# Kernel optimization log

Measured on AMD Instinct MI355X. Metric: run time of the kernel, lower is better.

Reference implementation:

```python
import jax, jax.numpy as jnp
import numpy as np

EPS = 1e-12

def _l2(v):
    return v / (jnp.linalg.norm(v) + EPS)

def _sn_weight(w, u):
    # Spectral normalization, one power iteration with stored u (not updated here).
    cout = w.shape[-1]
    wm = w.reshape(-1, cout)              # [d, cout]
    u = jax.lax.stop_gradient(u)
    v = _l2(wm @ u)                       # [d]
    u2 = _l2(wm.T @ v)                    # [cout]
    sigma = v @ (wm @ u2)
    return w / sigma

def _conv1x1(x, w, u):
    # 1x1 conv, no bias, with spectral-normalized kernel. x: [B,H,W,Cin], w: [1,1,Cin,Cout]
    wbar = _sn_weight(w, u)[0, 0]         # [Cin, Cout]
    return jnp.einsum('bhwc,co->bhwo', x, wbar)

def _maxpool2(x):
    # 2x2 max pool, stride 2, valid. x: [B,H,W,C]
    B, H, W, C = x.shape
    return x.reshape(B, H // 2, 2, W // 2, 2, C).max(axis=(2, 4))

def setup_inputs() -> dict:
    key = jax.random.key(0)
    ks = jax.random.split(key, 9)
    B, H, W, C = 16, 64, 64, 64
    inp = {
        'x': jax.random.normal(ks[0], (B, H, W, C), jnp.float32),
        'w_theta': jax.random.normal(ks[1], (1, 1, C, C // 8), jnp.float32) * 0.05,
        'u_theta': jax.random.normal(ks[2], (C // 8,), jnp.float32),
        'w_phi': jax.random.normal(ks[3], (1, 1, C, C // 8), jnp.float32) * 0.05,
        'u_phi': jax.random.normal(ks[4], (C // 8,), jnp.float32),
        'w_g': jax.random.normal(ks[5], (1, 1, C, C // 2), jnp.float32) * 0.05,
        'u_g': jax.random.normal(ks[6], (C // 2,), jnp.float32),
        'w_o': jax.random.normal(ks[7], (1, 1, C // 2, C), jnp.float32) * 0.05,
        'u_o': jax.random.normal(ks[8], (C,), jnp.float32),
        'gamma': jnp.zeros((1,), jnp.float32),
    }
    return inp

def reference(x, w_theta, u_theta, w_phi, u_phi, w_g, u_g, w_o, u_o, gamma):
    B, H, W, C = x.shape
    theta = _conv1x1(x, w_theta, u_theta).reshape(B, H * W, C // 8)          # [B,HW,C/8]
    phi = _maxpool2(_conv1x1(x, w_phi, u_phi)).reshape(B, H * W // 4, C // 8)  # [B,HW/4,C/8]
    attn = jax.nn.softmax(jnp.einsum('bnk,bmk->bnm', theta, phi), axis=-1)   # [B,HW,HW/4]
    g = _maxpool2(_conv1x1(x, w_g, u_g)).reshape(B, H * W // 4, C // 2)      # [B,HW/4,C/2]
    attn_g = jnp.einsum('bnm,bmc->bnc', attn, g).reshape(B, H, W, C // 2)    # [B,H,W,C/2]
    attn_g = _conv1x1(attn_g, w_o, u_o)                                      # [B,H,W,C]
    return x + gamma * attn_g
```

## Files before the change

kernel.cpp:

```cpp
#include <hip/hip_runtime.h>
#include <hip/hip_bf16.h>
#include <math.h>

#define NB 16
#define NPIX 4096
#define MPOOL 1024

typedef __attribute__((ext_vector_type(8))) short bf16x8;
typedef __attribute__((ext_vector_type(4))) float f32x4;

#define LOG2E 1.44269504088896340736f

__device__ inline unsigned short f2bf(float f) {
    __hip_bfloat16 h = __float2bfloat16(f);
    return *reinterpret_cast<unsigned short*>(&h);
}

#if defined(__has_builtin)
#if __has_builtin(__builtin_amdgcn_cvt_pk_bf16_f32)
#define HAVE_PK_BF16 1
#endif
#endif
__device__ inline unsigned pack_bf16(float a, float b) {
#ifdef HAVE_PK_BF16
    typedef __bf16 bf16v2 __attribute__((ext_vector_type(2)));
    bf16v2 v = __builtin_amdgcn_cvt_pk_bf16_f32(a, b);
    unsigned u;
    __builtin_memcpy(&u, &v, 4);
    return u;
#else
    unsigned ua = __float_as_uint(a) + 0x8000u;
    unsigned ub = __float_as_uint(b) + 0x8000u;
    return __builtin_amdgcn_perm(ua, ub, 0x03020706u);
#endif
}


__device__ inline float wave_sum64(float v) {
    #pragma unroll
    for (int off = 32; off >= 1; off >>= 1) v += __shfl_xor(v, off);
    return v;
}

template<int D, int COUT>
__device__ float sn_inv_sigma(const float* __restrict__ w, const float* __restrict__ u) {
    const int lane = threadIdx.x & 63;
    float vi = 0.f;
    if (lane < D) {
        #pragma unroll 8
        for (int j = 0; j < COUT; ++j) vi += w[lane * COUT + j] * u[j];
    }
    float nn = wave_sum64(vi * vi);
    vi *= 1.0f / (sqrtf(nn) + 1e-12f);

    float u2 = 0.f;
    #pragma unroll 8
    for (int i = 0; i < D; ++i) {
        float vv = __shfl(vi, i);
        if (lane < COUT) u2 += w[i * COUT + lane] * vv;
    }
    float nn2 = wave_sum64(u2 * u2);
    u2 *= 1.0f / (sqrtf(nn2) + 1e-12f);

    float ti = 0.f;
    #pragma unroll 8
    for (int j = 0; j < COUT; ++j) {
        float uv = __shfl(u2, j);
        if (lane < D) ti += w[lane * COUT + j] * uv;
    }
    float sig = wave_sum64(vi * ti);
    return 1.0f / sig;
}

__global__ __launch_bounds__(256) void conv_all_kernel(const float* __restrict__ x,
                                                       const float* __restrict__ w_theta, const float* __restrict__ u_theta,
                                                       const float* __restrict__ w_phi,   const float* __restrict__ u_phi,
                                                       const float* __restrict__ w_g,     const float* __restrict__ u_g,
                                                       const float* __restrict__ w_o,     const float* __restrict__ u_o,
                                                       unsigned short* __restrict__ theta_bf,
                                                       unsigned short* __restrict__ phi_bf,
                                                       unsigned short* __restrict__ gT_bf,
                                                       unsigned short* __restrict__ woT_bf) {
    __shared__ unsigned short sx[128 * 72];
    __shared__ unsigned short sw[48 * 72];
    __shared__ float s_inv[3];

    const int tid  = threadIdx.x;
    const int b    = blockIdx.x >> 5;
    const int hp   = blockIdx.x & 31;
    const int h0   = hp * 2;
    const int wv   = tid >> 6;
    const int lane = tid & 63;
    const int quad = lane >> 4;
    const int lcol = lane & 15;
    const int w0   = wv * 16;

    const float4* xb4 = (const float4*)(x + (((size_t)b * NPIX) + h0 * 64) * 64);
    #pragma unroll
    for (int it = 0; it < 8; ++it) {
        const int li = tid + it * 256;
        float4 v = xb4[li];
        const int px = li >> 4, c4 = li & 15;
        uint2 pk;
        pk.x = pack_bf16(v.x, v.y);
        pk.y = pack_bf16(v.z, v.w);
        *(uint2*)(&sx[px * 72 + c4 * 4]) = pk;
    }
    if (wv == 0)      { float iv = sn_inv_sigma<64, 8>(w_theta, u_theta); if (lane == 0) s_inv[0] = iv; }
    else if (wv == 1) { float iv = sn_inv_sigma<64, 8>(w_phi,   u_phi);   if (lane == 0) s_inv[1] = iv; }
    else if (wv == 2) { float iv = sn_inv_sigma<64, 32>(w_g,    u_g);     if (lane == 0) s_inv[2] = iv; }
    else if (blockIdx.x == 0) {
        float iv = sn_inv_sigma<32, 64>(w_o, u_o);
        for (int idx = lane; idx < 64 * 32; idx += 64) {
            const int n = idx >> 5, k = idx & 31;
            woT_bf[idx] = f2bf(w_o[k * 64 + n] * iv);
        }
    }
    __syncthreads();

    {
        const float i0 = s_inv[0], i1 = s_inv[1], i2 = s_inv[2];
        #pragma unroll
        for (int it = 0; it < 12; ++it) {
            const int idx = tid + it * 256;
            const int col = idx >> 6, k = idx & 63;
            float wvf, inv;
            if (col < 8)       { wvf = w_theta[k * 8 + col];        inv = i0; }
            else if (col < 16) { wvf = w_phi[k * 8 + (col - 8)];    inv = i1; }
            else               { wvf = w_g[k * 32 + (col - 16)];    inv = i2; }
            sw[col * 72 + k] = f2bf(wvf * inv);
        }
    }
    __syncthreads();

    bf16x8 a[2][2];
    #pragma unroll
    for (int hh = 0; hh < 2; ++hh)
        #pragma unroll
        for (int kc = 0; kc < 2; ++kc)
            a[hh][kc] = *(const bf16x8*)(sx + (hh * 64 + w0 + lcol) * 72 + kc * 32 + quad * 8);

    f32x4 acc[2][3];
    #pragma unroll
    for (int ct = 0; ct < 3; ++ct) {
        bf16x8 b0 = *(const bf16x8*)(sw + (ct * 16 + lcol) * 72 + 0 * 32 + quad * 8);
        bf16x8 b1 = *(const bf16x8*)(sw + (ct * 16 + lcol) * 72 + 1 * 32 + quad * 8);
        #pragma unroll
        for (int hh = 0; hh < 2; ++hh) {
            f32x4 c = __builtin_amdgcn_mfma_f32_16x16x32_bf16(a[hh][0], b0, (f32x4)0.0f, 0, 0, 0);
            acc[hh][ct] = __builtin_amdgcn_mfma_f32_16x16x32_bf16(a[hh][1], b1, c, 0, 0, 0);
        }
    }
    __syncthreads();

    unsigned short* th = sx;
    unsigned short* ph = sx + 1024;
    unsigned short* gg = sx + 1280;
    const int ml = (w0 >> 1) + quad * 2;
    if (lcol < 8) {
        #pragma unroll
        for (int hh = 0; hh < 2; ++hh) {
            const int pix = hh * 64 + w0 + quad * 4;
            #pragma unroll
            for (int r = 0; r < 4; ++r)
                th[(pix + r) * 8 + lcol] = f2bf(acc[hh][0][r] * LOG2E);
        }
    } else {
        #pragma unroll
        for (int r2 = 0; r2 < 2; ++r2) {
            float pe = fmaxf(fmaxf(acc[0][0][2 * r2], acc[0][0][2 * r2 + 1]),
                             fmaxf(acc[1][0][2 * r2], acc[1][0][2 * r2 + 1]));
            ph[(ml + r2) * 8 + (lcol - 8)] = f2bf(pe);
        }
    }
    #pragma unroll
    for (int ct = 1; ct < 3; ++ct) {
        const int cg = (ct - 1) * 16 + lcol;
        #pragma unroll
        for (int r2 = 0; r2 < 2; ++r2) {
            float pe = fmaxf(fmaxf(acc[0][ct][2 * r2], acc[0][ct][2 * r2 + 1]),
                             fmaxf(acc[1][ct][2 * r2], acc[1][ct][2 * r2 + 1]));
            gg[cg * 32 + ml + r2] = f2bf(pe);
        }
    }
    __syncthreads();

    const float4* sv4 = (const float4*)sx;
    float4* th4 = (float4*)(theta_bf + ((size_t)b * NPIX + hp * 128) * 8);
    float4* ph4 = (float4*)(phi_bf + ((size_t)b * MPOOL + hp * 32) * 8);
    for (int idx = tid; idx < 288; idx += 256) {
        float4 v = sv4[idx];
        if (idx < 128) {
            th4[idx] = v;
        } else if (idx < 160) {
            ph4[idx - 128] = v;
        } else {
            const int gi = idx - 160;
            const int ch = gi >> 2, part = gi & 3;
            *(float4*)(gT_bf + ((size_t)b * 32 + ch) * MPOOL + hp * 32 + part * 8) = v;
        }
    }
}

__global__ __launch_bounds__(512) void attn_kernel(const unsigned short* __restrict__ theta_bf,
                                                   const unsigned short* __restrict__ phi_bf,
                                                   const unsigned short* __restrict__ gT_bf,
                                                   const unsigned short* __restrict__ woT_bf,
                                                   const float* __restrict__ x,
                                                   const float* __restrict__ gamma,
                                                   float* __restrict__ out) {
    __shared__ unsigned short sphi[MPOOL * 8];
    __shared__ unsigned short sg[2][32 * 264];
    __shared__ unsigned short sP[8][16 * 72];
    __shared__ unsigned short swo[64 * 40];

    const int tid  = threadIdx.x;
    const int b    = blockIdx.x >> 5;
    const int qb   = blockIdx.x & 31;
    const int w    = tid >> 6;
    const int lane = tid & 63;
    const int quad = lane >> 4;
    const int lcol = lane & 15;

    {
        const float4* src = (const float4*)(phi_bf + (size_t)b * (MPOOL * 8));
        float4* dst = (float4*)sphi;
        dst[2 * tid]     = src[2 * tid];
        dst[2 * tid + 1] = src[2 * tid + 1];
    }
    {
        const int n = tid >> 3, ks = (tid & 7) * 4;
        *(uint2*)(swo + n * 40 + ks) = *(const uint2*)(woT_bf + n * 32 + ks);
    }
    const unsigned short* gTb = gT_bf + (size_t)b * (32 * MPOOL);
    const int prow = tid >> 4, pseg = tid & 15;
    {
        const float4* src = (const float4*)(gTb + prow * MPOOL + pseg * 16);
        float4 r0 = src[0], r1 = src[1];
        float4* dst = (float4*)(&sg[0][prow * 264 + pseg * 16]);
        dst[0] = r0; dst[1] = r1;
    }
    const int q0w = qb * 128 + w * 16;
    bf16x8 tfrag = (bf16x8)(short)0;
    if (quad == 0)
        tfrag = *(const bf16x8*)(theta_bf + ((size_t)b * NPIX + q0w + lcol) * 8);
    __syncthreads();

    f32x4 olo = (f32x4)0.0f, ohi = (f32x4)0.0f;
    float ls = 0.f;
    unsigned short* sPw = sP[w];

    float4 pre0, pre1;
    for (int t = 0; t < 4; ++t) {
        if (t < 3) {
            const float4* src = (const float4*)(gTb + prow * MPOOL + (t + 1) * 256 + pseg * 16);
            pre0 = src[0]; pre1 = src[1];
        }
        const unsigned short* sgb = sg[t & 1];
        for (int cb = 0; cb < 4; ++cb) {
            const int m0 = t * 256 + cb * 64;
            f32x4 s[4];
            #pragma unroll
            for (int sc = 0; sc < 4; ++sc) {
                bf16x8 pf = *(const bf16x8*)(sphi + (size_t)(m0 + sc * 16 + lcol) * 8);
                s[sc] = __builtin_amdgcn_mfma_f32_16x16x32_bf16(pf, tfrag, (f32x4)0.0f, 0, 0, 0);
            }
            #pragma unroll
            for (int sc = 0; sc < 4; ++sc) {
                float e0 = exp2f(s[sc][0]);
                float e1 = exp2f(s[sc][1]);
                float e2 = exp2f(s[sc][2]);
                float e3 = exp2f(s[sc][3]);
                ls += (e0 + e1) + (e2 + e3);
                uint2 pk2;
                pk2.x = pack_bf16(e0, e1);
                pk2.y = pack_bf16(e2, e3);
                *(uint2*)(sPw + lcol * 72 + sc * 16 + quad * 4) = pk2;
            }
            asm volatile("s_waitcnt lgkmcnt(0)" ::: "memory");
            #pragma unroll
            for (int pkk = 0; pkk < 2; ++pkk) {
                bf16x8 afrag = *(const bf16x8*)(sPw + lcol * 72 + pkk * 32 + quad * 8);
                bf16x8 bg0 = *(const bf16x8*)(sgb + lcol * 264 + cb * 64 + pkk * 32 + quad * 8);
                olo = __builtin_amdgcn_mfma_f32_16x16x32_bf16(afrag, bg0, olo, 0, 0, 0);
                bf16x8 bg1 = *(const bf16x8*)(sgb + (16 + lcol) * 264 + cb * 64 + pkk * 32 + quad * 8);
                ohi = __builtin_amdgcn_mfma_f32_16x16x32_bf16(afrag, bg1, ohi, 0, 0, 0);
            }
        }
        if (t < 3) {
            float4* dst = (float4*)(&sg[(t + 1) & 1][prow * 264 + pseg * 16]);
            dst[0] = pre0; dst[1] = pre1;
        }
        __syncthreads();
    }

    ls += __shfl_xor(ls, 16);
    ls += __shfl_xor(ls, 32);
    const float invq = 1.0f / ls;

    #pragma unroll
    for (int r = 0; r < 4; ++r) {
        sPw[(quad * 4 + r) * 40 + lcol]      = f2bf(olo[r]);
        sPw[(quad * 4 + r) * 40 + 16 + lcol] = f2bf(ohi[r]);
    }
    asm volatile("s_waitcnt lgkmcnt(0)" ::: "memory");
    bf16x8 agf = *(const bf16x8*)(sPw + lcol * 40 + quad * 8);

    const float gmi = gamma[0] * invq;
    const size_t pixbase = ((size_t)b * NPIX + q0w + lcol) * 64;
    #pragma unroll
    for (int ct = 0; ct < 4; ++ct) {
        bf16x8 wa = *(const bf16x8*)(swo + (ct * 16 + lcol) * 40 + quad * 8);
        f32x4 oc = __builtin_amdgcn_mfma_f32_16x16x32_bf16(wa, agf, (f32x4)0.0f, 0, 0, 0);
        const float4 xv = *(const float4*)(x + pixbase + ct * 16 + quad * 4);
        float4 ov;
        ov.x = xv.x + gmi * oc[0];
        ov.y = xv.y + gmi * oc[1];
        ov.z = xv.z + gmi * oc[2];
        ov.w = xv.w + gmi * oc[3];
        *(float4*)(out + pixbase + ct * 16 + quad * 4) = ov;
    }
}

extern "C" void kernel_launch(void* const* d_in, const int* in_sizes, int n_in,
                              void* d_out, int out_size, void* d_ws, size_t ws_size,
                              hipStream_t stream) {
    const float* x       = (const float*)d_in[0];
    const float* w_theta = (const float*)d_in[1];
    const float* u_theta = (const float*)d_in[2];
    const float* w_phi   = (const float*)d_in[3];
    const float* u_phi   = (const float*)d_in[4];
    const float* w_g     = (const float*)d_in[5];
    const float* u_g     = (const float*)d_in[6];
    const float* w_o     = (const float*)d_in[7];
    const float* u_o     = (const float*)d_in[8];
    const float* gamma   = (const float*)d_in[9];
    float* out = (float*)d_out;

    unsigned short* u16base  = (unsigned short*)d_ws;
    unsigned short* theta_bf = u16base;
    unsigned short* phi_bf   = u16base + 524288;
    unsigned short* gT_bf    = u16base + 655360;
    unsigned short* woT_bf   = u16base + 1179648;

    conv_all_kernel<<<512, 256, 0, stream>>>(x, w_theta, u_theta, w_phi, u_phi, w_g, u_g,
                                             w_o, u_o, theta_bf, phi_bf, gT_bf, woT_bf);
    attn_kernel<<<512, 512, 0, stream>>>(theta_bf, phi_bf, gT_bf, woT_bf, x, gamma, out);
}
```

Before: 120.4 us.

## Switch attention to 32x32x16 MFMA with permlane P reuse and full-g LDS

Rewrites the attention kernel to use 32x32x16 bf16 MFMA tiles, with 32 queries per wave and 256 queries per block, launching half as many blocks. The softmax probabilities go straight from the score accumulator into the PV MFMA operand through v_permlane32_swap, which drops the per-wave LDS round-trip for P. The whole g^T for the batch now loads into LDS at once instead of being double-buffered, and the output projection also uses 32x32 MFMAs. In exchange, the block uses more LDS, the grid of 256 blocks may underfill the GPU, and the big up-front g load is no longer overlapped with compute.

```diff
diff --git a/kernel.cpp b/kernel.cpp
--- a/kernel.cpp
+++ b/kernel.cpp
@@ -8,6 +8,7 @@
 
 typedef __attribute__((ext_vector_type(8))) short bf16x8;
 typedef __attribute__((ext_vector_type(4))) float f32x4;
+typedef __attribute__((ext_vector_type(16))) float f32x16;
 
 #define LOG2E 1.44269504088896340736f
 
@@ -210,17 +211,17 @@
                                                    const float* __restrict__ gamma,
                                                    float* __restrict__ out) {
     __shared__ unsigned short sphi[MPOOL * 8];
-    __shared__ unsigned short sg[2][32 * 264];
-    __shared__ unsigned short sP[8][16 * 72];
+    __shared__ unsigned short sg[32][1032];
     __shared__ unsigned short swo[64 * 40];
+    __shared__ unsigned short strans[8][32 * 40];
 
     const int tid  = threadIdx.x;
-    const int b    = blockIdx.x >> 5;
-    const int qb   = blockIdx.x & 31;
-    const int w    = tid >> 6;
+    const int b    = blockIdx.x >> 4;
+    const int qb   = blockIdx.x & 15;
+    const int wv   = tid >> 6;
     const int lane = tid & 63;
-    const int quad = lane >> 4;
-    const int lcol = lane & 15;
+    const int l31  = lane & 31;
+    const int half = lane >> 5;
 
     {
         const float4* src = (const float4*)(phi_bf + (size_t)b * (MPOOL * 8));
@@ -232,93 +233,84 @@
         const int n = tid >> 3, ks = (tid & 7) * 4;
         *(uint2*)(swo + n * 40 + ks) = *(const uint2*)(woT_bf + n * 32 + ks);
     }
-    const unsigned short* gTb = gT_bf + (size_t)b * (32 * MPOOL);
-    const int prow = tid >> 4, pseg = tid & 15;
     {
-        const float4* src = (const float4*)(gTb + prow * MPOOL + pseg * 16);
-        float4 r0 = src[0], r1 = src[1];
-        float4* dst = (float4*)(&sg[0][prow * 264 + pseg * 16]);
-        dst[0] = r0; dst[1] = r1;
-    }
-    const int q0w = qb * 128 + w * 16;
+        const unsigned short* gTb = gT_bf + (size_t)b * (32 * MPOOL);
+        const int r = tid >> 4, seg = tid & 15;
+        const float4* src = (const float4*)(gTb + r * MPOOL + seg * 64);
+        float4* dst = (float4*)(&sg[r][seg * 64]);
+        #pragma unroll
+        for (int j = 0; j < 8; ++j) dst[j] = src[j];
+    }
+    const int q0w = qb * 256 + wv * 32;
     bf16x8 tfrag = (bf16x8)(short)0;
-    if (quad == 0)
-        tfrag = *(const bf16x8*)(theta_bf + ((size_t)b * NPIX + q0w + lcol) * 8);
-    __syncthreads();
-
-    f32x4 olo = (f32x4)0.0f, ohi = (f32x4)0.0f;
+    if (half == 0)
+        tfrag = *(const bf16x8*)(theta_bf + ((size_t)b * NPIX + q0w + l31) * 8);
+    __syncthreads();
+
+    f32x16 acc = (f32x16)0.0f;
     float ls = 0.f;
-    unsigned short* sPw = sP[w];
-
-    float4 pre0, pre1;
-    for (int t = 0; t < 4; ++t) {
-        if (t < 3) {
-            const float4* src = (const float4*)(gTb + prow * MPOOL + (t + 1) * 256 + pseg * 16);
-            pre0 = src[0]; pre1 = src[1];
-        }
-        const unsigned short* sgb = sg[t & 1];
-        for (int cb = 0; cb < 4; ++cb) {
-            const int m0 = t * 256 + cb * 64;
-            f32x4 s[4];
-            #pragma unroll
-            for (int sc = 0; sc < 4; ++sc) {
-                bf16x8 pf = *(const bf16x8*)(sphi + (size_t)(m0 + sc * 16 + lcol) * 8);
-                s[sc] = __builtin_amdgcn_mfma_f32_16x16x32_bf16(pf, tfrag, (f32x4)0.0f, 0, 0, 0);
-            }
-            #pragma unroll
-            for (int sc = 0; sc < 4; ++sc) {
-                float e0 = exp2f(s[sc][0]);
-                float e1 = exp2f(s[sc][1]);
-                float e2 = exp2f(s[sc][2]);
-                float e3 = exp2f(s[sc][3]);
-                ls += (e0 + e1) + (e2 + e3);
-                uint2 pk2;
-                pk2.x = pack_bf16(e0, e1);
-                pk2.y = pack_bf16(e2, e3);
-                *(uint2*)(sPw + lcol * 72 + sc * 16 + quad * 4) = pk2;
-            }
-            asm volatile("s_waitcnt lgkmcnt(0)" ::: "memory");
-            #pragma unroll
-            for (int pkk = 0; pkk < 2; ++pkk) {
-                bf16x8 afrag = *(const bf16x8*)(sPw + lcol * 72 + pkk * 32 + quad * 8);
-                bf16x8 bg0 = *(const bf16x8*)(sgb + lcol * 264 + cb * 64 + pkk * 32 + quad * 8);
-                olo = __builtin_amdgcn_mfma_f32_16x16x32_bf16(afrag, bg0, olo, 0, 0, 0);
-                bf16x8 bg1 = *(const bf16x8*)(sgb + (16 + lcol) * 264 + cb * 64 + pkk * 32 + quad * 8);
-                ohi = __builtin_amdgcn_mfma_f32_16x16x32_bf16(afrag, bg1, ohi, 0, 0, 0);
-            }
-        }
-        if (t < 3) {
-            float4* dst = (float4*)(&sg[(t + 1) & 1][prow * 264 + pseg * 16]);
-            dst[0] = pre0; dst[1] = pre1;
-        }
-        __syncthreads();
-    }
-
-    ls += __shfl_xor(ls, 16);
+
+    for (int mt = 0; mt < 32; ++mt) {
+        const int m0 = mt * 32;
+        bf16x8 pa = *(const bf16x8*)(sphi + (size_t)(m0 + l31) * 8);
+        f32x16 S = __builtin_amdgcn_mfma_f32_32x32x16_bf16(pa, tfrag, (f32x16)0.0f, 0, 0, 0);
+        float e0  = exp2f(S[0]),  e1  = exp2f(S[1]),  e2  = exp2f(S[2]),  e3  = exp2f(S[3]);
+        float e4  = exp2f(S[4]),  e5  = exp2f(S[5]),  e6  = exp2f(S[6]),  e7  = exp2f(S[7]);
+        float e8  = exp2f(S[8]),  e9  = exp2f(S[9]),  e10 = exp2f(S[10]), e11 = exp2f(S[11]);
+        float e12 = exp2f(S[12]), e13 = exp2f(S[13]), e14 = exp2f(S[14]), e15 = exp2f(S[15]);
+        ls += (((e0 + e1) + (e2 + e3)) + ((e4 + e5) + (e6 + e7)))
+            + (((e8 + e9) + (e10 + e11)) + ((e12 + e13) + (e14 + e15)));
+        unsigned c0 = pack_bf16(e0, e1),   c1 = pack_bf16(e2, e3);
+        unsigned c2 = pack_bf16(e4, e5),   c3 = pack_bf16(e6, e7);
+        unsigned c4 = pack_bf16(e8, e9),   c5 = pack_bf16(e10, e11);
+        unsigned c6 = pack_bf16(e12, e13), c7 = pack_bf16(e14, e15);
+        asm("v_permlane32_swap_b32 %0, %1" : "+v"(c2), "+v"(c0));
+        asm("v_permlane32_swap_b32 %0, %1" : "+v"(c3), "+v"(c1));
+        asm("v_permlane32_swap_b32 %0, %1" : "+v"(c6), "+v"(c4));
+        asm("v_permlane32_swap_b32 %0, %1" : "+v"(c7), "+v"(c5));
+        unsigned f0[4] = {c0, c1, c2, c3};
+        bf16x8 p0; __builtin_memcpy(&p0, f0, 16);
+        bf16x8 gb0 = *(const bf16x8*)(&sg[l31][m0 + half * 8]);
+        acc = __builtin_amdgcn_mfma_f32_32x32x16_bf16(p0, gb0, acc, 0, 0, 0);
+        unsigned f1[4] = {c4, c5, c6, c7};
+        bf16x8 p1; __builtin_memcpy(&p1, f1, 16);
+        bf16x8 gb1 = *(const bf16x8*)(&sg[l31][m0 + 16 + half * 8]);
+        acc = __builtin_amdgcn_mfma_f32_32x32x16_bf16(p1, gb1, acc, 0, 0, 0);
+    }
+
     ls += __shfl_xor(ls, 32);
     const float invq = 1.0f / ls;
 
-    #pragma unroll
-    for (int r = 0; r < 4; ++r) {
-        sPw[(quad * 4 + r) * 40 + lcol]      = f2bf(olo[r]);
-        sPw[(quad * 4 + r) * 40 + 16 + lcol] = f2bf(ohi[r]);
+    unsigned short* st = &strans[wv][0];
+    #pragma unroll
+    for (int r = 0; r < 16; ++r) {
+        const int q = (r & 3) + 8 * (r >> 2) + 4 * half;
+        st[q * 40 + l31] = f2bf(acc[r]);
     }
     asm volatile("s_waitcnt lgkmcnt(0)" ::: "memory");
-    bf16x8 agf = *(const bf16x8*)(sPw + lcol * 40 + quad * 8);
 
     const float gmi = gamma[0] * invq;
-    const size_t pixbase = ((size_t)b * NPIX + q0w + lcol) * 64;
-    #pragma unroll
-    for (int ct = 0; ct < 4; ++ct) {
-        bf16x8 wa = *(const bf16x8*)(swo + (ct * 16 + lcol) * 40 + quad * 8);
-        f32x4 oc = __builtin_amdgcn_mfma_f32_16x16x32_bf16(wa, agf, (f32x4)0.0f, 0, 0, 0);
-        const float4 xv = *(const float4*)(x + pixbase + ct * 16 + quad * 4);
-        float4 ov;
-        ov.x = xv.x + gmi * oc[0];
-        ov.y = xv.y + gmi * oc[1];
-        ov.z = xv.z + gmi * oc[2];
-        ov.w = xv.w + gmi * oc[3];
-        *(float4*)(out + pixbase + ct * 16 + quad * 4) = ov;
+    const size_t pixbase = ((size_t)b * NPIX + q0w + l31) * 64;
+    #pragma unroll
+    for (int ct = 0; ct < 2; ++ct) {
+        f32x16 oc = (f32x16)0.0f;
+        #pragma unroll
+        for (int kc = 0; kc < 2; ++kc) {
+            bf16x8 wa = *(const bf16x8*)(swo + (ct * 32 + l31) * 40 + kc * 16 + half * 8);
+            bf16x8 ag = *(const bf16x8*)(st + l31 * 40 + kc * 16 + half * 8);
+            oc = __builtin_amdgcn_mfma_f32_32x32x16_bf16(wa, ag, oc, 0, 0, 0);
+        }
+        #pragma unroll
+        for (int r2 = 0; r2 < 4; ++r2) {
+            const int co = ct * 32 + 8 * r2 + 4 * half;
+            const float4 xv = *(const float4*)(x + pixbase + co);
+            float4 ov;
+            ov.x = xv.x + gmi * oc[4 * r2 + 0];
+            ov.y = xv.y + gmi * oc[4 * r2 + 1];
+            ov.z = xv.z + gmi * oc[4 * r2 + 2];
+            ov.w = xv.w + gmi * oc[4 * r2 + 3];
+            *(float4*)(out + pixbase + co) = ov;
+        }
     }
 }
 
@@ -345,5 +337,5 @@
 
     conv_all_kernel<<<512, 256, 0, stream>>>(x, w_theta, u_theta, w_phi, u_phi, w_g, u_g,
                                              w_o, u_o, theta_bf, phi_bf, gT_bf, woT_bf);
-    attn_kernel<<<512, 512, 0, stream>>>(theta_bf, phi_bf, gT_bf, woT_bf, x, gamma, out);
-}
+    attn_kernel<<<256, 512, 0, stream>>>(theta_bf, phi_bf, gT_bf, woT_bf, x, gamma, out);
+}
```

After: 122.2 us. No clear change (+1.5%).

## Use 1024-thread attention blocks with single-buffered g tile and global w_o reads

Applied to the files above, without the earlier changes.

Doubles the attention block to 16 waves covering 256 queries, so each batch's phi and g tiles are staged into shared memory by half as many blocks. The g tile goes from double-buffered to single-buffered, with two barriers per step around the refill. The w_o shared staging is removed and its fragments are read straight from global memory. This cuts redundant staging traffic and LDS footprint, but adds barrier stalls and leaves only 256 blocks to spread across the CUs.

```diff
diff --git a/kernel.cpp b/kernel.cpp
--- a/kernel.cpp
+++ b/kernel.cpp
@@ -202,21 +202,20 @@
     }
 }
 
-__global__ __launch_bounds__(512) void attn_kernel(const unsigned short* __restrict__ theta_bf,
-                                                   const unsigned short* __restrict__ phi_bf,
-                                                   const unsigned short* __restrict__ gT_bf,
-                                                   const unsigned short* __restrict__ woT_bf,
-                                                   const float* __restrict__ x,
-                                                   const float* __restrict__ gamma,
-                                                   float* __restrict__ out) {
+__global__ __launch_bounds__(1024) void attn_kernel(const unsigned short* __restrict__ theta_bf,
+                                                    const unsigned short* __restrict__ phi_bf,
+                                                    const unsigned short* __restrict__ gT_bf,
+                                                    const unsigned short* __restrict__ woT_bf,
+                                                    const float* __restrict__ x,
+                                                    const float* __restrict__ gamma,
+                                                    float* __restrict__ out) {
     __shared__ unsigned short sphi[MPOOL * 8];
-    __shared__ unsigned short sg[2][32 * 264];
-    __shared__ unsigned short sP[8][16 * 72];
-    __shared__ unsigned short swo[64 * 40];
+    __shared__ unsigned short sg[32 * 264];
+    __shared__ unsigned short sP[16][16 * 72];
 
     const int tid  = threadIdx.x;
-    const int b    = blockIdx.x >> 5;
-    const int qb   = blockIdx.x & 31;
+    const int b    = blockIdx.x >> 4;
+    const int qb   = blockIdx.x & 15;
     const int w    = tid >> 6;
     const int lane = tid & 63;
     const int quad = lane >> 4;
@@ -224,23 +223,15 @@
 
     {
         const float4* src = (const float4*)(phi_bf + (size_t)b * (MPOOL * 8));
-        float4* dst = (float4*)sphi;
-        dst[2 * tid]     = src[2 * tid];
-        dst[2 * tid + 1] = src[2 * tid + 1];
-    }
+        ((float4*)sphi)[tid] = src[tid];
+    }
+    const unsigned short* gTb = gT_bf + (size_t)b * (32 * MPOOL);
+    const int gr = tid >> 5, gseg = tid & 31;
     {
-        const int n = tid >> 3, ks = (tid & 7) * 4;
-        *(uint2*)(swo + n * 40 + ks) = *(const uint2*)(woT_bf + n * 32 + ks);
-    }
-    const unsigned short* gTb = gT_bf + (size_t)b * (32 * MPOOL);
-    const int prow = tid >> 4, pseg = tid & 15;
-    {
-        const float4* src = (const float4*)(gTb + prow * MPOOL + pseg * 16);
-        float4 r0 = src[0], r1 = src[1];
-        float4* dst = (float4*)(&sg[0][prow * 264 + pseg * 16]);
-        dst[0] = r0; dst[1] = r1;
-    }
-    const int q0w = qb * 128 + w * 16;
+        *(float4*)(&sg[gr * 264 + gseg * 8]) =
+            *(const float4*)(gTb + gr * MPOOL + gseg * 8);
+    }
+    const int q0w = qb * 256 + w * 16;
     bf16x8 tfrag = (bf16x8)(short)0;
     if (quad == 0)
         tfrag = *(const bf16x8*)(theta_bf + ((size_t)b * NPIX + q0w + lcol) * 8);
@@ -250,13 +241,10 @@
     float ls = 0.f;
     unsigned short* sPw = sP[w];
 
-    float4 pre0, pre1;
     for (int t = 0; t < 4; ++t) {
-        if (t < 3) {
-            const float4* src = (const float4*)(gTb + prow * MPOOL + (t + 1) * 256 + pseg * 16);
-            pre0 = src[0]; pre1 = src[1];
-        }
-        const unsigned short* sgb = sg[t & 1];
+        float4 pre;
+        if (t < 3)
+            pre = *(const float4*)(gTb + gr * MPOOL + (t + 1) * 256 + gseg * 8);
         for (int cb = 0; cb < 4; ++cb) {
             const int m0 = t * 256 + cb * 64;
             f32x4 s[4];
@@ -281,17 +269,17 @@
             #pragma unroll
             for (int pkk = 0; pkk < 2; ++pkk) {
                 bf16x8 afrag = *(const bf16x8*)(sPw + lcol * 72 + pkk * 32 + quad * 8);
-                bf16x8 bg0 = *(const bf16x8*)(sgb + lcol * 264 + cb * 64 + pkk * 32 + quad * 8);
+                bf16x8 bg0 = *(const bf16x8*)(sg + lcol * 264 + cb * 64 + pkk * 32 + quad * 8);
                 olo = __builtin_amdgcn_mfma_f32_16x16x32_bf16(afrag, bg0, olo, 0, 0, 0);
-                bf16x8 bg1 = *(const bf16x8*)(sgb + (16 + lcol) * 264 + cb * 64 + pkk * 32 + quad * 8);
+                bf16x8 bg1 = *(const bf16x8*)(sg + (16 + lcol) * 264 + cb * 64 + pkk * 32 + quad * 8);
                 ohi = __builtin_amdgcn_mfma_f32_16x16x32_bf16(afrag, bg1, ohi, 0, 0, 0);
             }
         }
         if (t < 3) {
-            float4* dst = (float4*)(&sg[(t + 1) & 1][prow * 264 + pseg * 16]);
-            dst[0] = pre0; dst[1] = pre1;
-        }
-        __syncthreads();
+            __syncthreads();
+            *(float4*)(&sg[gr * 264 + gseg * 8]) = pre;
+            __syncthreads();
+        }
     }
 
     ls += __shfl_xor(ls, 16);
@@ -310,7 +298,7 @@
     const size_t pixbase = ((size_t)b * NPIX + q0w + lcol) * 64;
     #pragma unroll
     for (int ct = 0; ct < 4; ++ct) {
-        bf16x8 wa = *(const bf16x8*)(swo + (ct * 16 + lcol) * 40 + quad * 8);
+        bf16x8 wa = *(const bf16x8*)(woT_bf + (ct * 16 + lcol) * 32 + quad * 8);
         f32x4 oc = __builtin_amdgcn_mfma_f32_16x16x32_bf16(wa, agf, (f32x4)0.0f, 0, 0, 0);
         const float4 xv = *(const float4*)(x + pixbase + ct * 16 + quad * 4);
         float4 ov;
@@ -345,5 +333,5 @@
 
     conv_all_kernel<<<512, 256, 0, stream>>>(x, w_theta, u_theta, w_phi, u_phi, w_g, u_g,
                                              w_o, u_o, theta_bf, phi_bf, gT_bf, woT_bf);
-    attn_kernel<<<512, 512, 0, stream>>>(theta_bf, phi_bf, gT_bf, woT_bf, x, gamma, out);
-}
+    attn_kernel<<<256, 1024, 0, stream>>>(theta_bf, phi_bf, gT_bf, woT_bf, x, gamma, out);
+}
```

Result: no change. 120.1 us (-0.3%).
